# Performance work log

Measured on AMD Instinct MI355X. Metric: run time of the kernel, lower is better.

## Reference

```python
import jax, jax.numpy as jnp
import numpy as np

B, G, N, C = 8, 16, 1024, 256


def setup_inputs() -> dict:
    key = jax.random.key(0)
    k1, k2, k3, k4, k5 = jax.random.split(key, 5)
    x = jax.random.normal(k1, (B, G, N, C), dtype=jnp.float32)
    vs = jax.random.normal(k2, (B, G, 1, N, 3), dtype=jnp.float32)
    s = 1.0 / np.sqrt(C)
    W_fc = jax.random.normal(k3, (C, C), dtype=jnp.float32) * s   # nn.Linear weight [out,in]
    b_fc = jax.random.normal(k4, (C,), dtype=jnp.float32) * s
    W_vn = jax.random.normal(k5, (C, C), dtype=jnp.float32) * s   # VNLinear weight [out,in], no bias
    return {"x": x, "vs": vs, "W_fc": W_fc, "b_fc": b_fc, "W_vn": W_vn}


def reference(x, vs, W_fc, b_fc, W_vn):
    # q = fc(x): [B,G,N,C]
    q = jnp.einsum('bgnc,oc->bgno', x, W_fc) + b_fc
    # softmax over the point dim N (torch dim=2)
    atten = jax.nn.softmax(q, axis=2)
    xw = atten * x  # [B,G,N,C]
    # torch: expand to [B,G,C,N,3] * vs then sum over N.
    # Equivalent contraction without materializing the 5D tensor:
    v = jnp.squeeze(vs, axis=2)  # [B,G,N,3]
    out = jnp.einsum('bgnc,bgnd->bgcd', xw, v)  # [B,G,C,3]
    # VNLinear: bias-free linear over channel dim, shared across the 3 vector comps
    return jnp.einsum('bgcd,oc->bgod', out, W_vn)  # [B,G,C,3]
```

## Files before the change

### kernel.cpp

```cpp
#include <hip/hip_runtime.h>
#include <hip/hip_bf16.h>


#define NQ 1024
#define CQ 256
#define RT 128
#define XS 136

typedef __attribute__((ext_vector_type(8))) short bf16x8;
typedef __attribute__((ext_vector_type(4))) float f32x4;

__device__ __forceinline__ ushort2 pk2(float a, float b) {
    __hip_bfloat162 h = __float22bfloat162_rn(make_float2(a, b));
    ushort2 r;
    __builtin_memcpy(&r, &h, sizeof(r));
    return r;
}
__device__ __forceinline__ float bf2f(ushort h) {
    union { unsigned u; float f; } v; v.u = ((unsigned)h) << 16;
    return v.f;
}

__global__ __launch_bounds__(256, 2)
void attn_pool_partial(const float* __restrict__ x, const float* __restrict__ vs,
                       const float* __restrict__ Wfc, float* __restrict__ ws) {
    __shared__ __align__(16) ushort xs[RT * XS];
    __shared__ __align__(16) float  vsm[RT * 3];

    const int t = threadIdx.x;
    const int id = blockIdx.x;
    const int ch = (id >> 3) & 1;
    const int rest = (id & 7) | ((id >> 4) << 3);
    const int bg = rest >> 3;
    const int nt = rest & 7;
    const int n0 = nt * RT;
    const int c0 = ch * 128;

    const int w = t >> 6, lane = t & 63;
    const int quad = lane >> 4, l16 = lane & 15;
    const int cstrip = w * 32;

    const float* xb = x + (size_t)bg * NQ * CQ;
    const float* vb = vs + (size_t)bg * NQ * 3;

    bf16x8 bf[2][4][2];
    {
        const int myc0 = c0 + cstrip + l16;
        #pragma unroll
        for (int kc = 0; kc < 2; ++kc) {
            const int chk = (kc == 0) ? (ch ^ 1) : ch;
            const int kb = chk * 128 + quad * 8;
            #pragma unroll
            for (int ks = 0; ks < 4; ++ks) {
                #pragma unroll
                for (int ci = 0; ci < 2; ++ci) {
                    const float* p = Wfc + (size_t)(myc0 + ci * 16) * CQ + kb + ks * 32;
                    float4 lo = *reinterpret_cast<const float4*>(p);
                    float4 hi = *reinterpret_cast<const float4*>(p + 4);
                    ushort2 p0 = pk2(lo.x, lo.y), p1 = pk2(lo.z, lo.w);
                    ushort2 p2 = pk2(hi.x, hi.y), p3 = pk2(hi.z, hi.w);
                    bf[kc][ks][ci] = (bf16x8){ (short)p0.x, (short)p0.y, (short)p1.x, (short)p1.y,
                                               (short)p2.x, (short)p2.y, (short)p3.x, (short)p3.y };
                }
            }
        }
    }

    if (t < 96) {
        reinterpret_cast<float4*>(vsm)[t] =
            reinterpret_cast<const float4*>(vb + (size_t)n0 * 3)[t];
    }

    f32x4 acc[8][2];
    #pragma unroll
    for (int m = 0; m < 8; ++m)
        #pragma unroll
        for (int ci = 0; ci < 2; ++ci) acc[m][ci] = (f32x4){0.f, 0.f, 0.f, 0.f};

    #pragma unroll
    for (int kc = 0; kc < 2; ++kc) {
        const int chk = (kc == 0) ? (ch ^ 1) : ch;
        const int kc0 = chk * 128;
        #pragma unroll
        for (int p = 0; p < 16; ++p) {
            int idx = p * 256 + t;
            int row = idx >> 5, k4 = idx & 31;
            float4 v4 = *reinterpret_cast<const float4*>(
                xb + (size_t)(n0 + row) * CQ + kc0 + k4 * 4);
            ushort2 a0 = pk2(v4.x, v4.y), a1 = pk2(v4.z, v4.w);
            ushort4 pk = { a0.x, a0.y, a1.x, a1.y };
            *reinterpret_cast<ushort4*>(&xs[row * XS + k4 * 4]) = pk;
        }
        __syncthreads();
        #pragma unroll
        for (int ks = 0; ks < 4; ++ks) {
            const int kk = ks * 32 + quad * 8;
            #pragma unroll
            for (int m = 0; m < 8; ++m) {
                bf16x8 a = *reinterpret_cast<const bf16x8*>(
                    &xs[(m * 16 + l16) * XS + kk]);
                acc[m][0] = __builtin_amdgcn_mfma_f32_16x16x32_bf16(a, bf[kc][ks][0], acc[m][0], 0, 0, 0);
                acc[m][1] = __builtin_amdgcn_mfma_f32_16x16x32_bf16(a, bf[kc][ks][1], acc[m][1], 0, 0, 0);
            }
        }
        if (kc == 0) __syncthreads();
    }

    float rZ[2] = {0.f, 0.f}, rS0[2] = {0.f, 0.f}, rS1[2] = {0.f, 0.f}, rS2[2] = {0.f, 0.f};
    #pragma unroll
    for (int m = 0; m < 8; ++m) {
        const int rbase = m * 16 + quad * 4;
        float v0[4], v1[4], v2[4];
        #pragma unroll
        for (int r = 0; r < 4; ++r) {
            v0[r] = vsm[(rbase + r) * 3 + 0];
            v1[r] = vsm[(rbase + r) * 3 + 1];
            v2[r] = vsm[(rbase + r) * 3 + 2];
        }
        #pragma unroll
        for (int ci = 0; ci < 2; ++ci) {
            const int xc = cstrip + ci * 16 + l16;
            #pragma unroll
            for (int r = 0; r < 4; ++r) {
                float e = __expf(acc[m][ci][r]);
                float xv = bf2f(xs[(rbase + r) * XS + xc]);
                rZ[ci] += e;
                float p = e * xv;
                rS0[ci] = fmaf(p, v0[r], rS0[ci]);
                rS1[ci] = fmaf(p, v1[r], rS1[ci]);
                rS2[ci] = fmaf(p, v2[r], rS2[ci]);
            }
        }
    }

    #pragma unroll
    for (int ci = 0; ci < 2; ++ci) {
        float z = rZ[ci], s0 = rS0[ci], s1 = rS1[ci], s2 = rS2[ci];
        #pragma unroll
        for (int off = 16; off < 64; off <<= 1) {
            z  += __shfl_xor(z,  off);
            s0 += __shfl_xor(s0, off);
            s1 += __shfl_xor(s1, off);
            s2 += __shfl_xor(s2, off);
        }
        if (quad == 0) {
            const int col = c0 + cstrip + ci * 16 + l16;
            float* p = ws + ((size_t)bg * CQ + col) * 4;
            atomicAdd(&p[0], z);
            atomicAdd(&p[1], s0);
            atomicAdd(&p[2], s1);
            atomicAdd(&p[3], s2);
        }
    }
}

__global__ __launch_bounds__(256, 4)
void vn_linear(const float* __restrict__ ws, const float* __restrict__ Wvn,
               float* __restrict__ out) {
    __shared__ float Tsm[CQ][3];
    const int bg = blockIdx.x, t = threadIdx.x;
    {
        f32x4 z4 = *reinterpret_cast<const f32x4*>(ws + ((size_t)bg * CQ + t) * 4);
        float inv = 1.f / z4[0];
        Tsm[t][0] = z4[1] * inv;
        Tsm[t][1] = z4[2] * inv;
        Tsm[t][2] = z4[3] * inv;
    }
    __syncthreads();
    const float* wr = Wvn + (size_t)t * CQ;
    float a0 = 0.f, a1 = 0.f, a2 = 0.f;
    #pragma unroll
    for (int c = 0; c < CQ; c += 4) {
        float4 w4 = *reinterpret_cast<const float4*>(wr + c);
        a0 += w4.x * Tsm[c + 0][0] + w4.y * Tsm[c + 1][0]
            + w4.z * Tsm[c + 2][0] + w4.w * Tsm[c + 3][0];
        a1 += w4.x * Tsm[c + 0][1] + w4.y * Tsm[c + 1][1]
            + w4.z * Tsm[c + 2][1] + w4.w * Tsm[c + 3][1];
        a2 += w4.x * Tsm[c + 0][2] + w4.y * Tsm[c + 1][2]
            + w4.z * Tsm[c + 2][2] + w4.w * Tsm[c + 3][2];
    }
    float* op = out + ((size_t)bg * CQ + t) * 3;
    op[0] = a0; op[1] = a1; op[2] = a2;
}

extern "C" void kernel_launch(void* const* d_in, const int* in_sizes, int n_in,
                              void* d_out, int out_size, void* d_ws, size_t ws_size,
                              hipStream_t stream) {
    const float* x   = (const float*)d_in[0];
    const float* vs  = (const float*)d_in[1];
    const float* Wfc = (const float*)d_in[2];
    const float* Wvn = (const float*)d_in[4];
    float* out = (float*)d_out;
    float* ws  = (float*)d_ws;

    (void)hipMemsetAsync(ws, 0, (size_t)128 * CQ * 4 * sizeof(float), stream);
    attn_pool_partial<<<dim3(2048), dim3(256), 0, stream>>>(x, vs, Wfc, ws);
    vn_linear<<<dim3(128), dim3(256), 0, stream>>>(ws, Wvn, out);
}
```

Measured before the change: 262.2 us.

## Pre-convert Wfc to bf16, halve row tile and raise occupancy

Adds a small pre-pass kernel that converts W_fc to bf16 once into workspace. The main kernel then loads bf16 B fragments inline from global instead of converting fp32 weights per block into registers. The row tile drops from 128 to 64, doubling the grid to 4096 blocks, and launch bounds rise to 4 blocks per CU. This cuts per-block register pressure and weight-conversion overhead, at the cost of more atomics, repeated weight reads and an extra launch.

```diff
diff --git a/kernel.cpp b/kernel.cpp
--- a/kernel.cpp
+++ b/kernel.cpp
@@ -4,8 +4,10 @@
 
 #define NQ 1024
 #define CQ 256
-#define RT 128
+#define RT 64
+#define NT 16
 #define XS 136
+#define WB_OFF 131072
 
 typedef __attribute__((ext_vector_type(8))) short bf16x8;
 typedef __attribute__((ext_vector_type(4))) float f32x4;
@@ -21,9 +23,18 @@
     return v.f;
 }
 
-__global__ __launch_bounds__(256, 2)
+__global__ __launch_bounds__(256)
+void wfc_cvt(const float* __restrict__ Wfc, ushort* __restrict__ Wb) {
+    const int i = blockIdx.x * 256 + threadIdx.x;
+    float4 v = reinterpret_cast<const float4*>(Wfc)[i];
+    ushort2 a0 = pk2(v.x, v.y), a1 = pk2(v.z, v.w);
+    ushort4 pk = { a0.x, a0.y, a1.x, a1.y };
+    reinterpret_cast<ushort4*>(Wb)[i] = pk;
+}
+
+__global__ __launch_bounds__(256, 4)
 void attn_pool_partial(const float* __restrict__ x, const float* __restrict__ vs,
-                       const float* __restrict__ Wfc, float* __restrict__ ws) {
+                       const ushort* __restrict__ Wb, float* __restrict__ ws) {
     __shared__ __align__(16) ushort xs[RT * XS];
     __shared__ __align__(16) float  vsm[RT * 3];
 
@@ -31,8 +42,8 @@
     const int id = blockIdx.x;
     const int ch = (id >> 3) & 1;
     const int rest = (id & 7) | ((id >> 4) << 3);
-    const int bg = rest >> 3;
-    const int nt = rest & 7;
+    const int bg = rest >> 4;
+    const int nt = rest & 15;
     const int n0 = nt * RT;
     const int c0 = ch * 128;
 
@@ -43,46 +54,25 @@
     const float* xb = x + (size_t)bg * NQ * CQ;
     const float* vb = vs + (size_t)bg * NQ * 3;
 
-    bf16x8 bf[2][4][2];
-    {
-        const int myc0 = c0 + cstrip + l16;
-        #pragma unroll
-        for (int kc = 0; kc < 2; ++kc) {
-            const int chk = (kc == 0) ? (ch ^ 1) : ch;
-            const int kb = chk * 128 + quad * 8;
-            #pragma unroll
-            for (int ks = 0; ks < 4; ++ks) {
-                #pragma unroll
-                for (int ci = 0; ci < 2; ++ci) {
-                    const float* p = Wfc + (size_t)(myc0 + ci * 16) * CQ + kb + ks * 32;
-                    float4 lo = *reinterpret_cast<const float4*>(p);
-                    float4 hi = *reinterpret_cast<const float4*>(p + 4);
-                    ushort2 p0 = pk2(lo.x, lo.y), p1 = pk2(lo.z, lo.w);
-                    ushort2 p2 = pk2(hi.x, hi.y), p3 = pk2(hi.z, hi.w);
-                    bf[kc][ks][ci] = (bf16x8){ (short)p0.x, (short)p0.y, (short)p1.x, (short)p1.y,
-                                               (short)p2.x, (short)p2.y, (short)p3.x, (short)p3.y };
-                }
-            }
-        }
-    }
-
-    if (t < 96) {
+    if (t < 48) {
         reinterpret_cast<float4*>(vsm)[t] =
             reinterpret_cast<const float4*>(vb + (size_t)n0 * 3)[t];
     }
 
-    f32x4 acc[8][2];
+    f32x4 acc[4][2];
     #pragma unroll
-    for (int m = 0; m < 8; ++m)
+    for (int m = 0; m < 4; ++m)
         #pragma unroll
         for (int ci = 0; ci < 2; ++ci) acc[m][ci] = (f32x4){0.f, 0.f, 0.f, 0.f};
+
+    const int bcol0 = c0 + cstrip + l16;
 
     #pragma unroll
     for (int kc = 0; kc < 2; ++kc) {
         const int chk = (kc == 0) ? (ch ^ 1) : ch;
         const int kc0 = chk * 128;
         #pragma unroll
-        for (int p = 0; p < 16; ++p) {
+        for (int p = 0; p < 8; ++p) {
             int idx = p * 256 + t;
             int row = idx >> 5, k4 = idx & 31;
             float4 v4 = *reinterpret_cast<const float4*>(
@@ -95,12 +85,16 @@
         #pragma unroll
         for (int ks = 0; ks < 4; ++ks) {
             const int kk = ks * 32 + quad * 8;
+            bf16x8 b0 = *reinterpret_cast<const bf16x8*>(
+                Wb + (size_t)bcol0 * CQ + kc0 + kk);
+            bf16x8 b1 = *reinterpret_cast<const bf16x8*>(
+                Wb + (size_t)(bcol0 + 16) * CQ + kc0 + kk);
             #pragma unroll
-            for (int m = 0; m < 8; ++m) {
+            for (int m = 0; m < 4; ++m) {
                 bf16x8 a = *reinterpret_cast<const bf16x8*>(
                     &xs[(m * 16 + l16) * XS + kk]);
-                acc[m][0] = __builtin_amdgcn_mfma_f32_16x16x32_bf16(a, bf[kc][ks][0], acc[m][0], 0, 0, 0);
-                acc[m][1] = __builtin_amdgcn_mfma_f32_16x16x32_bf16(a, bf[kc][ks][1], acc[m][1], 0, 0, 0);
+                acc[m][0] = __builtin_amdgcn_mfma_f32_16x16x32_bf16(a, b0, acc[m][0], 0, 0, 0);
+                acc[m][1] = __builtin_amdgcn_mfma_f32_16x16x32_bf16(a, b1, acc[m][1], 0, 0, 0);
             }
         }
         if (kc == 0) __syncthreads();
@@ -108,7 +102,7 @@
 
     float rZ[2] = {0.f, 0.f}, rS0[2] = {0.f, 0.f}, rS1[2] = {0.f, 0.f}, rS2[2] = {0.f, 0.f};
     #pragma unroll
-    for (int m = 0; m < 8; ++m) {
+    for (int m = 0; m < 4; ++m) {
         const int rbase = m * 16 + quad * 4;
         float v0[4], v1[4], v2[4];
         #pragma unroll
@@ -193,7 +187,10 @@
     float* out = (float*)d_out;
     float* ws  = (float*)d_ws;
 
+    ushort* Wb = (ushort*)(ws + WB_OFF);
+
     (void)hipMemsetAsync(ws, 0, (size_t)128 * CQ * 4 * sizeof(float), stream);
-    attn_pool_partial<<<dim3(2048), dim3(256), 0, stream>>>(x, vs, Wfc, ws);
+    wfc_cvt<<<dim3(64), dim3(256), 0, stream>>>(Wfc, Wb);
+    attn_pool_partial<<<dim3(4096), dim3(256), 0, stream>>>(x, vs, Wb, ws);
     vn_linear<<<dim3(128), dim3(256), 0, stream>>>(ws, Wvn, out);
 }
```

Measured after the change: 252.2 us. -3.8%, faster.
